# Performance work log

Measured on AMD Instinct MI355X. Metric: run time of the kernel, lower is better.

Reference implementation:

```python
import jax, jax.numpy as jnp
import numpy as np

B, D, L, T, K = 16, 256, 256, 1000, 3
DW, DC = 4, 2  # dim_w, dim_c
CH = 8         # ConvSwishBlock out channels (10 = 1 start + 1 end + 8)


def swish(x):
    return x * jax.nn.sigmoid(x)


def setup_inputs() -> dict:
    key = jax.random.key(0)
    ks = jax.random.split(key, 12)
    # durations ~ U[1,6] per phone -> sum ~ 3.5*L ~ 896 <= T
    durations = 1.0 + 5.0 * jax.random.uniform(ks[0], (B, L), dtype=jnp.float32)
    phoneme = jax.random.normal(ks[1], (B, D, L), dtype=jnp.float32)
    # True = padded phone position
    phone_len = L - (jnp.arange(B) % 4) * 16
    phoneme_mask = (jnp.arange(L)[None, :] >= phone_len[:, None])[:, None, :]
    durations = jnp.where(phoneme_mask[:, 0, :], 0.0, durations)
    s = 0.02
    p = {
        'proj_w_W': s * jax.random.normal(ks[2], (D, D)), 'proj_w_b': jnp.zeros((D,)),
        'conv_w_W': s * jax.random.normal(ks[3], (CH, D, K)), 'conv_w_b': jnp.zeros((CH,)),
        'mlp_w_W': s * jax.random.normal(ks[4], (2 + CH, DW)), 'mlp_w_b': jnp.zeros((DW,)),
        'lin_w_W': s * jax.random.normal(ks[5], (D * DW, D)), 'lin_w_b': jnp.zeros((D,)),
        'proj_c_W': s * jax.random.normal(ks[6], (D, D)), 'proj_c_b': jnp.zeros((D,)),
        'conv_c_W': s * jax.random.normal(ks[7], (CH, D, K)), 'conv_c_b': jnp.zeros((CH,)),
        'mlp_c_W': s * jax.random.normal(ks[8], (2 + CH, DC)), 'mlp_c_b': jnp.zeros((DC,)),
        'lin_c_W': s * jax.random.normal(ks[9], (DW * DC, D)), 'lin_c_b': jnp.zeros((D,)),
    }
    return {'durations': durations, 'phoneme': phoneme, 'phoneme_mask': phoneme_mask, **p}


def _conv_branch(x, phone_pad, projW, projb, convW, convb):
    # x: (B, D, L). 1x1 conv projection, then K-wide 'same' conv to CH channels, swish, mask.
    x = jnp.einsum('od,bdl->bol', projW, x) + projb[None, :, None]
    h = jax.lax.conv_general_dilated(x, convW, (1,), 'SAME',
                                     dimension_numbers=('NCH', 'OIH', 'NCH'))
    h = swish(h + convb[None, :, None])
    h = jnp.where(phone_pad[:, None, :], 0.0, h)
    return h.transpose(0, 2, 1)  # (B, L, CH)


def _forward(durations, phoneme, phoneme_mask,
             proj_w_W, proj_w_b, conv_w_W, conv_w_b, mlp_w_W, mlp_w_b, lin_w_W, lin_w_b,
             proj_c_W, proj_c_b, conv_c_W, conv_c_b, mlp_c_W, mlp_c_b, lin_c_W, lin_c_b):
    phone_pad = phoneme_mask[:, 0, :]                       # (B, L) True = pad
    frame_len = jnp.clip(jnp.round(jnp.sum(durations, -1)), 0, T).astype(jnp.int32)
    frame_pad = jnp.arange(T)[None, :] >= frame_len[:, None]  # (B, T) True = pad
    attn_pad = frame_pad[:, :, None] | phone_pad[:, None, :]  # (B, T, L)

    sd = jnp.cumsum(durations, -1)                          # (B, L) cumulative end times
    sk = sd - durations                                     # (B, L) start times
    t = jnp.arange(1, T + 1, dtype=durations.dtype)
    S = jnp.where(attn_pad, 0.0, t[None, :, None] - sk[:, None, :])                    # (B,T,L)
    E = jnp.where(attn_pad, 0.0, jnp.broadcast_to(sd[:, None, :], attn_pad.shape)
                  - sk[:, None, :])                                                    # (B,T,L)

    # W branch: per-(frame, phone) attention weights over phones
    h_w = _conv_branch(phoneme, phone_pad, proj_w_W, proj_w_b, conv_w_W, conv_w_b)     # (B,L,CH)
    feat_w = jnp.concatenate(
        [S[..., None], E[..., None], jnp.broadcast_to(h_w[:, None], (B, T, L, CH))], -1)
    w = swish(feat_w @ mlp_w_W + mlp_w_b)                   # (B, T, L, DW)
    w = jnp.where(phone_pad[:, None, :, None], -jnp.inf, w)
    w = jax.nn.softmax(w, axis=2)                           # softmax over phones
    w = jnp.where(frame_pad[:, :, None, None], 0.0, w)

    # C branch: auxiliary per-(frame, phone) context
    h_c = _conv_branch(phoneme, phone_pad, proj_c_W, proj_c_b, conv_c_W, conv_c_b)
    feat_c = jnp.concatenate(
        [S[..., None], E[..., None], jnp.broadcast_to(h_c[:, None], (B, T, L, CH))], -1)
    c = swish(feat_c @ mlp_c_W + mlp_c_b)                   # (B, T, L, DC)

    # combine: wh = einsum over phones with phoneme features, wc with c matrix
    wh = jnp.einsum('btnq,bnh->btqh', w, phoneme.transpose(0, 2, 1))  # (B,T,DW,D)
    wh = wh.reshape(B, T, DW * D) @ lin_w_W + lin_w_b                 # (B,T,D)
    wc = jnp.einsum('btnq,btnp->btqp', w, c)                          # (B,T,DW,DC)
    wc = wc.reshape(B, T, DW * DC) @ lin_c_W + lin_c_b                # (B,T,D)
    return wh + wc


def reference(durations, phoneme, phoneme_mask,
              proj_w_W, proj_w_b, conv_w_W, conv_w_b, mlp_w_W, mlp_w_b, lin_w_W, lin_w_b,
              proj_c_W, proj_c_b, conv_c_W, conv_c_b, mlp_c_W, mlp_c_b, lin_c_W, lin_c_b):
    return _forward(durations, phoneme, phoneme_mask,
                    proj_w_W, proj_w_b, conv_w_W, conv_w_b, mlp_w_W, mlp_w_b, lin_w_W, lin_w_b,
                    proj_c_W, proj_c_b, conv_c_W, conv_c_b, mlp_c_W, mlp_c_b, lin_c_W, lin_c_b)
```

## Files before the change

kernel.cpp:

```cpp
#include <hip/hip_runtime.h>


typedef short v8s __attribute__((ext_vector_type(8)));
typedef _Float16 v8h __attribute__((ext_vector_type(8)));
typedef float f4 __attribute__((ext_vector_type(4)));

__device__ __forceinline__ float bf2f(unsigned short h) {
  return __uint_as_float(((unsigned int)h) << 16);
}
__device__ __forceinline__ unsigned short f2bf(float f) {
  unsigned int u = __float_as_uint(f);
  u = (u + 0x7FFFu + ((u >> 16) & 1u)) >> 16;
  return (unsigned short)u;
}
__device__ __forceinline__ float swishf(float x) {
  return x * __builtin_amdgcn_rcpf(1.f + __expf(-x));
}

__global__ __launch_bounds__(256) void k_prep(
    const float* __restrict__ dur, const float* __restrict__ ph,
    const float* __restrict__ liWw,
    const float* __restrict__ cvWw, const float* __restrict__ pjWw,
    const float* __restrict__ pjbw,
    const float* __restrict__ cvWc, const float* __restrict__ pjWc,
    const float* __restrict__ pjbc,
    float* __restrict__ sk, int* __restrict__ frame_len,
    unsigned short* __restrict__ Mb, float* __restrict__ bK,
    unsigned short* __restrict__ LWT, unsigned short* __restrict__ phT) {
  __shared__ float sm[32 * 33];
  int blk = blockIdx.x, tid = threadIdx.x;
  if (blk < 16) {
    int b = blk, l = tid;
    float d = dur[b * 256 + l];
    sm[l] = d;
    __syncthreads();
    for (int off = 1; off < 256; off <<= 1) {
      float v = (l >= off) ? sm[l - off] : 0.f;
      __syncthreads();
      sm[l] += v;
      __syncthreads();
    }
    sk[b * 256 + l] = sm[l] - d;
    if (l == 255) {
      int fl = (int)rintf(sm[255]);
      frame_len[b] = min(max(fl, 0), 1000);
    }
  } else if (blk < 64) {
    int x = blk - 16;
    int br = x / 24, ck = x % 24;
    int ch = ck / 3, k = ck % 3;
    const float* convW = br ? cvWc : cvWw;
    const float* projW = br ? pjWc : pjWw;
    const float* projb = br ? pjbc : pjbw;
    int d = tid;
    float a0 = 0.f, a1 = 0.f, a2 = 0.f, a3 = 0.f;
    for (int o = 0; o < 256; o += 4) {
      a0 += convW[ch * 768 + (o + 0) * 3 + k] * projW[(o + 0) * 256 + d];
      a1 += convW[ch * 768 + (o + 1) * 3 + k] * projW[(o + 1) * 256 + d];
      a2 += convW[ch * 768 + (o + 2) * 3 + k] * projW[(o + 2) * 256 + d];
      a3 += convW[ch * 768 + (o + 3) * 3 + k] * projW[(o + 3) * 256 + d];
    }
    Mb[(br * 24 + ck) * 256 + d] = f2bf((a0 + a1) + (a2 + a3));
    if (tid < 64) {
      float pb = 0.f;
      for (int o = tid; o < 256; o += 64)
        pb += convW[ch * 768 + o * 3 + k] * projb[o];
#pragma unroll
      for (int off = 1; off < 64; off <<= 1) pb += __shfl_xor(pb, off);
      if (tid == 0) bK[br * 24 + ck] = pb;
    }
  } else if (blk < 320) {
    int idx = blk - 64;
    int kt = idx & 31, ot = idx >> 5;
    int tx = tid & 31, ty = tid >> 5;
#pragma unroll
    for (int r = 0; r < 4; r++) {
      int row = ty + r * 8;
      sm[row * 33 + tx] = liWw[(size_t)(kt * 32 + row) * 256 + ot * 32 + tx];
    }
    __syncthreads();
#pragma unroll
    for (int r = 0; r < 4; r++) {
      int row = ty + r * 8;
      LWT[(size_t)(ot * 32 + row) * 1024 + kt * 32 + tx] =
          f2bf(sm[tx * 33 + row]);
    }
  } else {
    int idx = blk - 320;
    int ht = idx & 7, lt = (idx >> 3) & 7, b = idx >> 6;
    int tx = tid & 31, ty = tid >> 5;
#pragma unroll
    for (int r = 0; r < 4; r++) {
      int row = ty + r * 8;
      sm[row * 33 + tx] =
          ph[(size_t)b * 65536 + (size_t)(ht * 32 + row) * 256 + lt * 32 + tx];
    }
    __syncthreads();
#pragma unroll
    for (int r = 0; r < 4; r++) {
      int row = ty + r * 8;
      phT[(size_t)b * 65536 + (size_t)(lt * 32 + row) * 256 + ht * 32 + tx] =
          f2bf(sm[tx * 33 + row]);
    }
  }
}

__global__ __launch_bounds__(256) void k_convG(
    const unsigned short* __restrict__ phT, const unsigned short* __restrict__ Mb,
    const float* __restrict__ bK, const float* __restrict__ cvbw,
    const float* __restrict__ cvbc, const float* __restrict__ dur,
    const float* __restrict__ sk, const float* __restrict__ mlpWw,
    const float* __restrict__ mlpbw, const float* __restrict__ mlpWc,
    const float* __restrict__ mlpbc, const unsigned short* __restrict__ LWT,
    float* __restrict__ Lbw, float* __restrict__ Laux,
    float* __restrict__ maxAb, _Float16* __restrict__ G) {
  __shared__ __align__(16) float C[256 * 49];
  __shared__ float redm[4][4];
  int blk = blockIdx.x;
  int tid = threadIdx.x, wave = tid >> 6, lane = tid & 63;
  int quad = lane >> 4, col = lane & 15;
  if (blk < 16) {
    int b = blk;
    int l0 = wave * 64;
    const unsigned short* Ab = phT + (size_t)b * 65536;
    f4 acc[4][3] = {};
#pragma unroll
    for (int k0 = 0; k0 < 256; k0 += 32) {
      v8s af[4], bf[3];
#pragma unroll
      for (int lt = 0; lt < 4; lt++)
        af[lt] = *(const v8s*)(Ab + (size_t)(l0 + lt * 16 + col) * 256 + k0 + quad * 8);
#pragma unroll
      for (int ct = 0; ct < 3; ct++)
        bf[ct] = *(const v8s*)(Mb + (size_t)(ct * 16 + col) * 256 + k0 + quad * 8);
#pragma unroll
      for (int lt = 0; lt < 4; lt++)
#pragma unroll
        for (int ct = 0; ct < 3; ct++)
          acc[lt][ct] = __builtin_amdgcn_mfma_f32_16x16x32_bf16(af[lt], bf[ct],
                                                                acc[lt][ct], 0, 0, 0);
    }
#pragma unroll
    for (int lt = 0; lt < 4; lt++)
#pragma unroll
      for (int ct = 0; ct < 3; ct++)
#pragma unroll
        for (int r = 0; r < 4; r++)
          C[(l0 + lt * 16 + quad * 4 + r) * 49 + ct * 16 + col] = acc[lt][ct][r];
    __syncthreads();
    int l = tid;
    float dv = dur[b * 256 + l];
    bool vld = (dv != 0.f);
    float hv[2][8];
#pragma unroll
    for (int br = 0; br < 2; br++) {
      const float* convb = br ? cvbc : cvbw;
#pragma unroll
      for (int ch = 0; ch < 8; ch++) {
        int ck = br * 24 + ch * 3;
        float v = convb[ch] + bK[ck + 1] + C[l * 49 + ck + 1];
        if (l > 0) v += bK[ck + 0] + C[(l - 1) * 49 + ck + 0];
        if (l < 255) v += bK[ck + 2] + C[(l + 1) * 49 + ck + 2];
        hv[br][ch] = vld ? swishf(v) : 0.f;
      }
    }
    float skl = sk[b * 256 + l];
    float A[4];
#pragma unroll
    for (int q = 0; q < 4; q++) {
      float a = mlpbw[q] + dv * mlpWw[4 + q] - skl * mlpWw[q];
#pragma unroll
      for (int ch = 0; ch < 8; ch++) a += hv[0][ch] * mlpWw[(2 + ch) * 4 + q];
      A[q] = vld ? a : -1e30f;
    }
    float bb0 = mlpbc[0] + dv * mlpWc[2] - skl * mlpWc[0];
    float bb1 = mlpbc[1] + dv * mlpWc[3] - skl * mlpWc[1];
#pragma unroll
    for (int ch = 0; ch < 8; ch++) {
      bb0 += hv[1][ch] * mlpWc[(2 + ch) * 2 + 0];
      bb1 += hv[1][ch] * mlpWc[(2 + ch) * 2 + 1];
    }
    float4 Av = {A[0], A[1], A[2], A[3]};
    ((float4*)Lbw)[b * 256 + l] = Av;
    float4 Xv = {bb0, bb1, vld ? 1.f : 0.f, 0.f};
    ((float4*)Laux)[b * 256 + l] = Xv;
    float m0 = A[0], m1 = A[1], m2 = A[2], m3 = A[3];
#pragma unroll
    for (int off = 1; off < 64; off <<= 1) {
      m0 = fmaxf(m0, __shfl_xor(m0, off));
      m1 = fmaxf(m1, __shfl_xor(m1, off));
      m2 = fmaxf(m2, __shfl_xor(m2, off));
      m3 = fmaxf(m3, __shfl_xor(m3, off));
    }
    if (lane == 0) {
      redm[wave][0] = m0;
      redm[wave][1] = m1;
      redm[wave][2] = m2;
      redm[wave][3] = m3;
    }
    __syncthreads();
    if (tid < 4)
      maxAb[b * 4 + tid] = fmaxf(fmaxf(redm[0][tid], redm[1][tid]),
                                 fmaxf(redm[2][tid], redm[3][tid]));
  } else {
    int idx = blk - 16;
    int b = idx >> 5;
    int sub = idx & 31;
    int q = sub >> 3, rem = sub & 7;
    int mo = (rem >> 2) * 128, nl = (rem & 3) * 64;
    int wm = (wave & 1) * 64, wn = (wave >> 1) * 32;
    const unsigned short* Ag = LWT + (size_t)q * 256;
    const unsigned short* Bg = phT + (size_t)b * 65536;
    f4 acc[4][2] = {};
#pragma unroll
    for (int k0 = 0; k0 < 256; k0 += 32) {
      v8s af[4], bf[2];
#pragma unroll
      for (int mt = 0; mt < 4; mt++)
        af[mt] = *(const v8s*)(Ag + (size_t)(mo + wm + mt * 16 + col) * 1024 +
                               k0 + quad * 8);
#pragma unroll
      for (int nt = 0; nt < 2; nt++)
        bf[nt] = *(const v8s*)(Bg + (size_t)(nl + wn + nt * 16 + col) * 256 +
                               k0 + quad * 8);
#pragma unroll
      for (int mt = 0; mt < 4; mt++)
#pragma unroll
        for (int nt = 0; nt < 2; nt++)
          acc[mt][nt] = __builtin_amdgcn_mfma_f32_16x16x32_bf16(af[mt], bf[nt],
                                                                acc[mt][nt], 0, 0, 0);
    }
    _Float16* Gb = G + (size_t)b * 262144 + q * 256;
#pragma unroll
    for (int mt = 0; mt < 4; mt++)
#pragma unroll
      for (int r = 0; r < 4; r++) {
        int orow = mo + wm + mt * 16 + quad * 4 + r;
#pragma unroll
        for (int nt = 0; nt < 2; nt++) {
          int lcol = nl + wn + nt * 16 + col;
          Gb[(size_t)orow * 1024 + lcol] = (_Float16)acc[mt][nt][r];
        }
      }
  }
}

__global__ __launch_bounds__(512, 4) void k_fuse(
    const float* __restrict__ Lbw, const float* __restrict__ Laux,
    const float* __restrict__ maxAb, const int* __restrict__ frame_len,
    const float* __restrict__ mlpWw, const float* __restrict__ mlpWc,
    const _Float16* __restrict__ G, const float* __restrict__ lwb,
    const float* __restrict__ lcb, const float* __restrict__ LC,
    float* __restrict__ out) {
  __shared__ __align__(16) _Float16 Asm[32 * 512];
  __shared__ __align__(16) float4 Lb4[272];
  __shared__ __align__(16) float4 Lx4[272];
  __shared__ float bias_s[256];
  __shared__ float lcs[8][256];
  __shared__ float wcs[32][8];

  int idx = blockIdx.x;
  int b = (idx & 7) * 2 + ((idx >> 3) & 1);
  int t0 = (idx >> 4) * 32;
  int tid = threadIdx.x, wave = tid >> 6, lane = tid & 63;
  int quad = lane >> 4, col = lane & 15;

  int fl = frame_len[b];
  if (t0 >= fl) {
    int o = tid & 255;
    float v = lwb[o] + lcb[o];
    for (int r = tid >> 8; r < 32; r += 2) {
      int t = t0 + r;
      if (t < 1000) out[((size_t)(b * 1000 + t)) * 256 + o] = v;
    }
    return;
  }

  if (tid < 256) {
    float4 av = ((const float4*)Lbw)[b * 256 + tid];
    float4 xv = ((const float4*)Laux)[b * 256 + tid];
    int li = tid + (tid >> 4);
    Lb4[li] = av;
    Lx4[li] = xv;
    bias_s[tid] = lwb[tid] + lcb[tid];
  }
  for (int i = tid; i < 2048; i += 512) lcs[i >> 8][i & 255] = LC[i];

  float4 mx4 = ((const float4*)maxAb)[b];
  float mw0 = mlpWw[0], mw1 = mlpWw[1], mw2 = mlpWw[2], mw3 = mlpWw[3];
  float mc0 = mlpWc[0], mc1 = mlpWc[1];

  int l_grp = lane & 15;
  int row = wave * 4 + (lane >> 4);
  int t = t0 + row;
  bool live = (t < fl);
  float tp1 = (float)(t + 1);
  int rsw = row & 7;
  int asw = col & 7;
  int wn = wave * 32;
  f4 acc[2][2] = {};

  __syncthreads();

  float cpa[16], cpb[16];
#pragma unroll
  for (int j = 0; j < 16; ++j) {
    int l = l_grp * 16 + j;
    int li = l + (l >> 4);
    float4 ax = Lx4[li];
    cpa[j] = swishf(ax.x + tp1 * mc0);
    cpb[j] = swishf(ax.y + tp1 * mc1);
  }

#pragma unroll
  for (int p = 0; p < 2; ++p) {
    if (p) __syncthreads();
    float mq0 = p ? mw2 : mw0;
    float mq1 = p ? mw3 : mw1;
    float mxa = p ? mx4.z : mx4.x;
    float mxb = p ? mx4.w : mx4.y;
    float m0 = live ? fmaxf(mxa + tp1 * mq0, 0.f) : 1e30f;
    float m1 = live ? fmaxf(mxb + tp1 * mq1, 0.f) : 1e30f;
    float s0 = 0.f, s1 = 0.f, p00 = 0.f, p01 = 0.f, p10 = 0.f, p11 = 0.f;
    v8h e0[2], e1[2];
#pragma unroll
    for (int j = 0; j < 16; ++j) {
      int l = l_grp * 16 + j;
      int li = l + (l >> 4);
      float4 A4 = Lb4[li];
      float zz = ((const float*)&Lx4[li])[2];
      float Aq0 = p ? A4.z : A4.x;
      float Aq1 = p ? A4.w : A4.y;
      _Float16 eh0 = (_Float16)(__expf(swishf(Aq0 + tp1 * mq0) - m0) * zz);
      _Float16 eh1 = (_Float16)(__expf(swishf(Aq1 + tp1 * mq1) - m1) * zz);
      e0[j >> 3][j & 7] = eh0;
      e1[j >> 3][j & 7] = eh1;
      float f0 = (float)eh0, f1 = (float)eh1;
      s0 += f0;
      s1 += f1;
      p00 += f0 * cpa[j];
      p01 += f0 * cpb[j];
      p10 += f1 * cpa[j];
      p11 += f1 * cpb[j];
    }
#pragma unroll
    for (int off = 1; off < 16; off <<= 1) {
      s0 += __shfl_xor(s0, off);
      s1 += __shfl_xor(s1, off);
      p00 += __shfl_xor(p00, off);
      p01 += __shfl_xor(p01, off);
      p10 += __shfl_xor(p10, off);
      p11 += __shfl_xor(p11, off);
    }
    float iv0 = live ? 1.0f / s0 : 0.f;
    float iv1 = live ? 1.0f / s1 : 0.f;
    if (l_grp == 0) {
      wcs[row][p * 4 + 0] = p00 * iv0;
      wcs[row][p * 4 + 1] = p01 * iv0;
      wcs[row][p * 4 + 2] = p10 * iv1;
      wcs[row][p * 4 + 3] = p11 * iv1;
    }
#pragma unroll
    for (int c = 0; c < 2; ++c) {
      int sl = (l_grp * 2 + c) ^ rsw;
      v8h w0, w1;
#pragma unroll
      for (int k = 0; k < 8; ++k) {
        w0[k] = (_Float16)((float)e0[c][k] * iv0);
        w1[k] = (_Float16)((float)e1[c][k] * iv1);
      }
      *(v8h*)&Asm[(row * 64 + sl) * 8] = w0;
      *(v8h*)&Asm[(row * 64 + 32 + sl) * 8] = w1;
    }
    __syncthreads();
    const _Float16* Gp = G + (size_t)b * 262144 + p * 512;
    __builtin_amdgcn_s_setprio(1);
#pragma unroll 2
    for (int k0 = 0; k0 < 512; k0 += 32) {
      int slk = (k0 >> 3) + quad;
      v8h af[2], bf[2];
#pragma unroll
      for (int mt = 0; mt < 2; ++mt)
        af[mt] = *(const v8h*)&Asm[((mt * 16 + col) * 64 + (slk ^ asw)) * 8];
#pragma unroll
      for (int nt = 0; nt < 2; ++nt)
        bf[nt] =
            *(const v8h*)(Gp + (size_t)(wn + nt * 16 + col) * 1024 + k0 + quad * 8);
#pragma unroll
      for (int mt = 0; mt < 2; ++mt)
#pragma unroll
        for (int nt = 0; nt < 2; ++nt)
          acc[mt][nt] = __builtin_amdgcn_mfma_f32_16x16x32_f16(af[mt], bf[nt],
                                                               acc[mt][nt], 0, 0, 0);
    }
    __builtin_amdgcn_s_setprio(0);
  }
#pragma unroll
  for (int mt = 0; mt < 2; ++mt)
#pragma unroll
    for (int r = 0; r < 4; ++r) {
      int lrow = mt * 16 + quad * 4 + r;
      int trow = t0 + lrow;
      if (trow < 1000) {
        float4 wa = *(const float4*)&wcs[lrow][0];
        float4 wb = *(const float4*)&wcs[lrow][4];
        float wcl[8] = {wa.x, wa.y, wa.z, wa.w, wb.x, wb.y, wb.z, wb.w};
#pragma unroll
        for (int nt = 0; nt < 2; ++nt) {
          int oc = wn + nt * 16 + col;
          float v = acc[mt][nt][r] + bias_s[oc];
#pragma unroll
          for (int jj = 0; jj < 8; ++jj) v = fmaf(wcl[jj], lcs[jj][oc], v);
          out[((size_t)(b * 1000 + trow)) * 256 + oc] = v;
        }
      }
    }
}

extern "C" void kernel_launch(void* const* d_in, const int* in_sizes, int n_in,
                              void* d_out, int out_size, void* d_ws, size_t ws_size,
                              hipStream_t stream) {
  const float* dur  = (const float*)d_in[0];
  const float* ph   = (const float*)d_in[1];
  const float* pjWw = (const float*)d_in[3];
  const float* pjbw = (const float*)d_in[4];
  const float* cvWw = (const float*)d_in[5];
  const float* cvbw = (const float*)d_in[6];
  const float* mlWw = (const float*)d_in[7];
  const float* mlbw = (const float*)d_in[8];
  const float* liWw = (const float*)d_in[9];
  const float* libw = (const float*)d_in[10];
  const float* pjWc = (const float*)d_in[11];
  const float* pjbc = (const float*)d_in[12];
  const float* cvWc = (const float*)d_in[13];
  const float* cvbc = (const float*)d_in[14];
  const float* mlWc = (const float*)d_in[15];
  const float* mlbc = (const float*)d_in[16];
  const float* liWc = (const float*)d_in[17];
  const float* libc = (const float*)d_in[18];
  float* out = (float*)d_out;

  float* f = (float*)d_ws;
  size_t o = 0;
  float* sk = f + o;            o += 4096;
  int* fl = (int*)(f + o);      o += 16;
  float* bK = f + o;            o += 64;
  unsigned short* Mb = (unsigned short*)(f + o); o += 6144;
  float* Lbw = f + o;           o += 16384;
  float* Laux = f + o;          o += 16384;
  float* mxA = f + o;           o += 64;
  _Float16* G = (_Float16*)(f + o);              o += 2097152;
  unsigned short* phT = (unsigned short*)(f + o); o += 524288;
  unsigned short* LWT = (unsigned short*)(f + o); o += 131072;

  k_prep<<<1344, 256, 0, stream>>>(dur, ph, liWw, cvWw, pjWw, pjbw, cvWc, pjWc,
                                   pjbc, sk, fl, Mb, bK, LWT, phT);
  k_convG<<<528, 256, 0, stream>>>(phT, Mb, bK, cvbw, cvbc, dur, sk, mlWw,
                                   mlbw, mlWc, mlbc, LWT, Lbw, Laux, mxA, G);
  k_fuse<<<512, 512, 0, stream>>>(Lbw, Laux, mxA, fl, mlWw, mlWc, G, libw,
                                  libc, liWc, out);
}
```

Baseline: 177.8 us.

## Software-pipeline global operand loads in prep GEMM and fused MFMA loop

In the prep GEMM, the weight and phoneme fragments are double-buffered in registers so the next k-step's global loads are issued while the current MFMAs run. The block-to-batch mapping is also reordered to interleave batches across consecutive blocks. In the fused kernel, the first four G fragments for each pass are prefetched before the softmax/exp computation and kept as a 4-deep rolling register buffer through a fully unrolled MFMA loop. The second-pass barrier is moved after the reductions. This hides global-load latency behind compute at the cost of more registers, which may reduce occupancy under launch_bounds(512,4).

```diff
diff --git a/kernel.cpp b/kernel.cpp
--- a/kernel.cpp
+++ b/kernel.cpp
@@ -204,31 +204,48 @@
                                  fmaxf(redm[2][tid], redm[3][tid]));
   } else {
     int idx = blk - 16;
-    int b = idx >> 5;
-    int sub = idx & 31;
+    int b = (idx & 7) * 2 + ((idx >> 3) & 1);
+    int sub = idx >> 4;
     int q = sub >> 3, rem = sub & 7;
     int mo = (rem >> 2) * 128, nl = (rem & 3) * 64;
     int wm = (wave & 1) * 64, wn = (wave >> 1) * 32;
     const unsigned short* Ag = LWT + (size_t)q * 256;
     const unsigned short* Bg = phT + (size_t)b * 65536;
+    size_t aoff[4], boff[2];
+#pragma unroll
+    for (int mt = 0; mt < 4; mt++)
+      aoff[mt] = (size_t)(mo + wm + mt * 16 + col) * 1024 + quad * 8;
+#pragma unroll
+    for (int nt = 0; nt < 2; nt++)
+      boff[nt] = (size_t)(nl + wn + nt * 16 + col) * 256 + quad * 8;
+
+    v8s ra[2][4], rb[2][2];
+#pragma unroll
+    for (int c = 0; c < 2; c++) {
+#pragma unroll
+      for (int mt = 0; mt < 4; mt++)
+        ra[c][mt] = *(const v8s*)(Ag + aoff[mt] + c * 32);
+#pragma unroll
+      for (int nt = 0; nt < 2; nt++)
+        rb[c][nt] = *(const v8s*)(Bg + boff[nt] + c * 32);
+    }
     f4 acc[4][2] = {};
 #pragma unroll
-    for (int k0 = 0; k0 < 256; k0 += 32) {
-      v8s af[4], bf[2];
+    for (int s = 0; s < 8; s++) {
 #pragma unroll
       for (int mt = 0; mt < 4; mt++)
-        af[mt] = *(const v8s*)(Ag + (size_t)(mo + wm + mt * 16 + col) * 1024 +
-                               k0 + quad * 8);
-#pragma unroll
-      for (int nt = 0; nt < 2; nt++)
-        bf[nt] = *(const v8s*)(Bg + (size_t)(nl + wn + nt * 16 + col) * 256 +
-                               k0 + quad * 8);
-#pragma unroll
-      for (int mt = 0; mt < 4; mt++)
 #pragma unroll
         for (int nt = 0; nt < 2; nt++)
-          acc[mt][nt] = __builtin_amdgcn_mfma_f32_16x16x32_bf16(af[mt], bf[nt],
-                                                                acc[mt][nt], 0, 0, 0);
+          acc[mt][nt] = __builtin_amdgcn_mfma_f32_16x16x32_bf16(
+              ra[s & 1][mt], rb[s & 1][nt], acc[mt][nt], 0, 0, 0);
+      if (s < 6) {
+#pragma unroll
+        for (int mt = 0; mt < 4; mt++)
+          ra[s & 1][mt] = *(const v8s*)(Ag + aoff[mt] + (s + 2) * 32);
+#pragma unroll
+        for (int nt = 0; nt < 2; nt++)
+          rb[s & 1][nt] = *(const v8s*)(Bg + boff[nt] + (s + 2) * 32);
+      }
     }
     _Float16* Gb = G + (size_t)b * 262144 + q * 256;
 #pragma unroll
@@ -300,6 +317,10 @@
   int wn = wave * 32;
   f4 acc[2][2] = {};
 
+  const _Float16* GA =
+      G + (size_t)b * 262144 + (size_t)(wn + col) * 1024 + quad * 8;
+  const _Float16* GB = GA + (size_t)16 * 1024;
+
   __syncthreads();
 
   float cpa[16], cpb[16];
@@ -314,7 +335,15 @@
 
 #pragma unroll
   for (int p = 0; p < 2; ++p) {
-    if (p) __syncthreads();
+    const _Float16* GpA = GA + p * 512;
+    const _Float16* GpB = GB + p * 512;
+    v8h rb[4][2];
+#pragma unroll
+    for (int c = 0; c < 4; ++c) {
+      rb[c][0] = *(const v8h*)(GpA + c * 32);
+      rb[c][1] = *(const v8h*)(GpB + c * 32);
+    }
+
     float mq0 = p ? mw2 : mw0;
     float mq1 = p ? mw3 : mw1;
     float mxa = p ? mx4.z : mx4.x;
@@ -354,6 +383,9 @@
     }
     float iv0 = live ? 1.0f / s0 : 0.f;
     float iv1 = live ? 1.0f / s1 : 0.f;
+
+    if (p) __syncthreads();
+
     if (l_grp == 0) {
       wcs[row][p * 4 + 0] = p00 * iv0;
       wcs[row][p * 4 + 1] = p01 * iv0;
@@ -373,25 +405,24 @@
       *(v8h*)&Asm[(row * 64 + 32 + sl) * 8] = w1;
     }
     __syncthreads();
-    const _Float16* Gp = G + (size_t)b * 262144 + p * 512;
     __builtin_amdgcn_s_setprio(1);
-#pragma unroll 2
-    for (int k0 = 0; k0 < 512; k0 += 32) {
-      int slk = (k0 >> 3) + quad;
-      v8h af[2], bf[2];
-#pragma unroll
-      for (int mt = 0; mt < 2; ++mt)
-        af[mt] = *(const v8h*)&Asm[((mt * 16 + col) * 64 + (slk ^ asw)) * 8];
-#pragma unroll
-      for (int nt = 0; nt < 2; ++nt)
-        bf[nt] =
-            *(const v8h*)(Gp + (size_t)(wn + nt * 16 + col) * 1024 + k0 + quad * 8);
-#pragma unroll
-      for (int mt = 0; mt < 2; ++mt)
-#pragma unroll
-        for (int nt = 0; nt < 2; ++nt)
-          acc[mt][nt] = __builtin_amdgcn_mfma_f32_16x16x32_f16(af[mt], bf[nt],
-                                                               acc[mt][nt], 0, 0, 0);
+#pragma unroll
+    for (int s = 0; s < 16; ++s) {
+      int slk = s * 4 + quad;
+      v8h af0 = *(const v8h*)&Asm[(col * 64 + (slk ^ asw)) * 8];
+      v8h af1 = *(const v8h*)&Asm[((16 + col) * 64 + (slk ^ asw)) * 8];
+      acc[0][0] = __builtin_amdgcn_mfma_f32_16x16x32_f16(af0, rb[s & 3][0],
+                                                         acc[0][0], 0, 0, 0);
+      acc[1][0] = __builtin_amdgcn_mfma_f32_16x16x32_f16(af1, rb[s & 3][0],
+                                                         acc[1][0], 0, 0, 0);
+      acc[0][1] = __builtin_amdgcn_mfma_f32_16x16x32_f16(af0, rb[s & 3][1],
+                                                         acc[0][1], 0, 0, 0);
+      acc[1][1] = __builtin_amdgcn_mfma_f32_16x16x32_f16(af1, rb[s & 3][1],
+                                                         acc[1][1], 0, 0, 0);
+      if (s < 12) {
+        rb[s & 3][0] = *(const v8h*)(GpA + (s + 4) * 32);
+        rb[s & 3][1] = *(const v8h*)(GpB + (s + 4) * 32);
+      }
     }
     __builtin_amdgcn_s_setprio(0);
   }
```

After: 180.3 us. No clear change (+1.4%).
